# Kernel tuning notes

Hardware: AMD Instinct MI355X
Metric: run time of the kernel (lower is better)

The kernel has to match this reference:

```python
import jax, jax.numpy as jnp
import numpy as np

N_NODES = 50000
N_EDGES = 800000
D = 128
N_LAYERS = 3  # n_layers=2 -> 3 attention layers


def setup_inputs() -> dict:
    key = jax.random.key(0)
    ks = jax.random.split(key, 7)
    x = jax.random.normal(ks[0], (N_NODES, D), dtype=jnp.float32)
    edge_src = jax.random.randint(ks[1], (N_EDGES,), 0, N_NODES)
    edge_dst = jax.random.randint(ks[2], (N_EDGES,), 0, N_NODES)
    # Linear weights stored as [in, out] (equivalent to torch W.T)
    lin_w = jax.random.normal(ks[3], (N_LAYERS, D, D), dtype=jnp.float32) / np.sqrt(D)
    lin_b = jax.random.normal(ks[4], (N_LAYERS, D), dtype=jnp.float32) * 0.01
    attn_w = jax.random.normal(ks[5], (N_LAYERS, 2 * D), dtype=jnp.float32) / np.sqrt(2 * D)
    attn_b = jax.random.normal(ks[6], (N_LAYERS,), dtype=jnp.float32) * 0.01
    return {"x": x, "edge_src": edge_src, "edge_dst": edge_dst,
            "lin_w": lin_w, "lin_b": lin_b, "attn_w": attn_w, "attn_b": attn_b}


def reference(x, edge_src, edge_dst, lin_w, lin_b, attn_w, attn_b):
    n = x.shape[0]
    h = x
    for l in range(N_LAYERS):
        # h = leaky_relu(linear(x), 0.2)
        h = jax.nn.leaky_relu(h @ lin_w[l] + lin_b[l], negative_slope=0.2)
        f = h.shape[1]
        # e_ij = attn(cat(h_i, h_j)) -> split the attn weight into left/right halves
        s_left = h @ attn_w[l, :f]   # [N]
        s_right = h @ attn_w[l, f:]  # [N]
        e = s_left[edge_src] + s_right[edge_dst] + attn_b[l]  # [E]
        # sparse softmax over dim=1: normalize per source row i
        m = jax.ops.segment_max(e, edge_src, num_segments=n)
        ex = jnp.exp(e - m[edge_src])
        denom = jax.ops.segment_sum(ex, edge_src, num_segments=n)
        alpha = ex / denom[edge_src]  # [E]
        # h2[i] += h[j] * alpha_ij
        h2 = jax.ops.segment_sum(h[edge_dst] * alpha[:, None], edge_src, num_segments=n)
        h = jax.nn.relu(h2)  # self.activation
    return h
```

## Files before the change

### kernel.cpp

```cpp
#include <hip/hip_runtime.h>
#include <math.h>

#define N_NODES 50000
#define N_EDGES 800000
#define D 128
#define N_LAYERS 3

#define FCHUNK 2048
#define NCHUNK ((N_EDGES + FCHUNK - 1) / FCHUNK)
#define GDIV 6250
#define SLOT 96
#define PREPB ((N_LAYERS * D * D) / 256)
#define LINB ((N_NODES + 63) / 64)

typedef _Float16 half8 __attribute__((ext_vector_type(8)));
typedef _Float16 half4 __attribute__((ext_vector_type(4)));
typedef float f32x4 __attribute__((ext_vector_type(4)));

__global__ __launch_bounds__(256) void prep_w_kernel(
    const float* __restrict__ W, _Float16* __restrict__ Wt)
{
    int idx = blockIdx.x * 256 + threadIdx.x;
    int l = idx >> 14, rem = idx & (D * D - 1);
    int k = rem >> 7, n = rem & 127;
    Wt[l * D * D + n * D + k] = (_Float16)W[idx];
}

template <bool F32IN, bool FUSEFILL>
__global__ __launch_bounds__(256) void linear_mfma_kernel(
    const void* __restrict__ Ain, const _Float16* __restrict__ Wt,
    const float* __restrict__ b, const float* __restrict__ awr,
    _Float16* __restrict__ hout, float* __restrict__ sr,
    const int* __restrict__ esrc, const int* __restrict__ edst,
    int* __restrict__ cnt, unsigned short* __restrict__ csr16)
{
    __shared__ _Float16 Wl[D * 130];

    if (FUSEFILL && blockIdx.x >= LINB) {
        int fi = blockIdx.x - LINB;
        int g = blockIdx.x & 7;
        int base = (fi >> 3) * FCHUNK;
        int ecnt = N_EDGES - base;
        if (ecnt > FCHUNK) ecnt = FCHUNK;
        unsigned glo = (unsigned)(g * GDIV);
        for (int i = threadIdx.x * 4; i < ecnt; i += 1024) {
            int4 s4 = *(const int4*)(esrc + base + i);
            int4 d4 = *(const int4*)(edst + base + i);
            int ss[4] = {s4.x, s4.y, s4.z, s4.w};
            int dd[4] = {d4.x, d4.y, d4.z, d4.w};
#pragma unroll
            for (int j = 0; j < 4; ++j) {
                if ((unsigned)ss[j] - glo < (unsigned)GDIV) {
                    int pos = atomicAdd(cnt + ss[j], 1);
                    if (pos < SLOT)
                        csr16[(size_t)ss[j] * SLOT + pos] = (unsigned short)dd[j];
                }
            }
        }
        return;
    }

    int tid = threadIdx.x;
    for (int j = tid * 8; j < D * D; j += 2048) {
        int n = j >> 7, k = j & 127;
        *(half8*)(&Wl[n * 130 + k]) = *(const half8*)(Wt + j);
    }
    __syncthreads();

    int wid = tid >> 6, lane = tid & 63;
    int m = lane & 15, q = lane >> 4;
    int rowbase = blockIdx.x * 64 + wid * 16;
    int row = rowbase + m;

    half8 a[4];
    if (row < N_NODES) {
        if (F32IN) {
            const float* ar = (const float*)Ain + (size_t)row * D;
#pragma unroll
            for (int s = 0; s < 4; ++s) {
                float4 lo = *(const float4*)(ar + s * 32 + q * 8);
                float4 hi = *(const float4*)(ar + s * 32 + q * 8 + 4);
                a[s][0] = (_Float16)lo.x; a[s][1] = (_Float16)lo.y;
                a[s][2] = (_Float16)lo.z; a[s][3] = (_Float16)lo.w;
                a[s][4] = (_Float16)hi.x; a[s][5] = (_Float16)hi.y;
                a[s][6] = (_Float16)hi.z; a[s][7] = (_Float16)hi.w;
            }
        } else {
            const _Float16* ar = (const _Float16*)Ain + (size_t)row * D;
#pragma unroll
            for (int s = 0; s < 4; ++s)
                a[s] = *(const half8*)(ar + s * 32 + q * 8);
        }
    } else {
#pragma unroll
        for (int s = 0; s < 4; ++s)
#pragma unroll
            for (int j = 0; j < 8; ++j) a[s][j] = (_Float16)0.f;
    }

    f32x4 acc[8];
#pragma unroll
    for (int t = 0; t < 8; ++t) acc[t] = (f32x4)(0.f);

#pragma unroll
    for (int s = 0; s < 4; ++s) {
#pragma unroll
        for (int t = 0; t < 8; ++t) {
            half8 bf = *(const half8*)(&Wl[(t * 16 + m) * 130 + s * 32 + q * 8]);
            acc[t] = __builtin_amdgcn_mfma_f32_16x16x32_f16(a[s], bf, acc[t], 0, 0, 0);
        }
    }

    float sp[4] = {0.f, 0.f, 0.f, 0.f};
#pragma unroll
    for (int t = 0; t < 8; ++t) {
        int col = t * 16 + m;
        float bc = b[col];
        float ac = awr[col];
#pragma unroll
        for (int r = 0; r < 4; ++r) {
            int orow = rowbase + q * 4 + r;
            float v = acc[t][r] + bc;
            v = v > 0.f ? v : 0.2f * v;
            sp[r] = fmaf(v, ac, sp[r]);
            if (orow < N_NODES)
                hout[(size_t)orow * D + col] = (_Float16)v;
        }
    }
#pragma unroll
    for (int r = 0; r < 4; ++r) {
#pragma unroll
        for (int o = 1; o < 16; o <<= 1)
            sp[r] += __shfl_xor(sp[r], o, 64);
    }
    if (m == 0) {
#pragma unroll
        for (int r = 0; r < 4; ++r) {
            int orow = rowbase + q * 4 + r;
            if (orow < N_NODES) sr[orow] = sp[r];
        }
    }
}

__global__ __launch_bounds__(256, 8) void gather_kernel(
    const int* __restrict__ cnt, const unsigned short* __restrict__ csr16,
    const float* __restrict__ sr, const _Float16* __restrict__ h,
    _Float16* __restrict__ out16, float* __restrict__ out32)
{
    __shared__ int plds[4][2 * SLOT + 8];
    int wid = threadIdx.x >> 6, lane = threadIdx.x & 63;
    int half = lane >> 5, sl = lane & 31;
    int n = blockIdx.x * 4 + wid;
    int deg = cnt[n];
    if (deg > SLOT) deg = SLOT;
    const unsigned short* ce = csr16 + (size_t)n * SLOT;
    int* prow = plds[wid];

    float ev[2];
    float m = -INFINITY;
#pragma unroll
    for (int t = 0; t < 2; ++t) {
        int k = t * 64 + lane;
        if (k < deg) {
            int d = ce[k];
            prow[2 * k] = d << 8;
            float e = sr[d];
            ev[t] = e;
            m = fmaxf(m, e);
        }
    }
    for (int o = 32; o > 0; o >>= 1) m = fmaxf(m, __shfl_xor(m, o, 64));

    float s = 0.f;
#pragma unroll
    for (int t = 0; t < 2; ++t) {
        int k = t * 64 + lane;
        if (k < deg) {
            float a = __expf(ev[t] - m);
            prow[2 * k + 1] = __float_as_int(a);
            s += a;
        }
    }
    for (int o = 32; o > 0; o >>= 1) s += __shfl_xor(s, o, 64);
    float inv = (deg > 0) ? 1.f / s : 0.f;

    float acc0 = 0.f, acc1 = 0.f, acc2 = 0.f, acc3 = 0.f;
    const char* hb = (const char*)h + sl * 8;
    int k = 0;
    int deg8 = deg & ~7;
    for (; k < deg8; k += 8) {
        int2 p0 = *(const int2*)(prow + 2 * (k + half));
        int2 p1 = *(const int2*)(prow + 2 * (k + 2 + half));
        int2 p2 = *(const int2*)(prow + 2 * (k + 4 + half));
        int2 p3 = *(const int2*)(prow + 2 * (k + 6 + half));
        half4 h0 = *(const half4*)(hb + p0.x);
        half4 h1 = *(const half4*)(hb + p1.x);
        half4 h2 = *(const half4*)(hb + p2.x);
        half4 h3 = *(const half4*)(hb + p3.x);
        float a0 = __int_as_float(p0.y);
        float a1 = __int_as_float(p1.y);
        float a2 = __int_as_float(p2.y);
        float a3 = __int_as_float(p3.y);
        acc0 = fmaf((float)h0[0], a0, acc0);
        acc1 = fmaf((float)h0[1], a0, acc1);
        acc2 = fmaf((float)h0[2], a0, acc2);
        acc3 = fmaf((float)h0[3], a0, acc3);
        acc0 = fmaf((float)h1[0], a1, acc0);
        acc1 = fmaf((float)h1[1], a1, acc1);
        acc2 = fmaf((float)h1[2], a1, acc2);
        acc3 = fmaf((float)h1[3], a1, acc3);
        acc0 = fmaf((float)h2[0], a2, acc0);
        acc1 = fmaf((float)h2[1], a2, acc1);
        acc2 = fmaf((float)h2[2], a2, acc2);
        acc3 = fmaf((float)h2[3], a2, acc3);
        acc0 = fmaf((float)h3[0], a3, acc0);
        acc1 = fmaf((float)h3[1], a3, acc1);
        acc2 = fmaf((float)h3[2], a3, acc2);
        acc3 = fmaf((float)h3[3], a3, acc3);
    }
    for (; k < deg; k += 2) {
        int kk = k + half;
        int2 p = (kk < deg) ? *(const int2*)(prow + 2 * kk) : make_int2(0, 0);
        half4 hv = *(const half4*)(hb + p.x);
        float a = __int_as_float(p.y);
        acc0 = fmaf((float)hv[0], a, acc0);
        acc1 = fmaf((float)hv[1], a, acc1);
        acc2 = fmaf((float)hv[2], a, acc2);
        acc3 = fmaf((float)hv[3], a, acc3);
    }

    acc0 += __shfl_xor(acc0, 32, 64);
    acc1 += __shfl_xor(acc1, 32, 64);
    acc2 += __shfl_xor(acc2, 32, 64);
    acc3 += __shfl_xor(acc3, 32, 64);

    if (half == 0) {
        float r0 = fmaxf(acc0 * inv, 0.f);
        float r1 = fmaxf(acc1 * inv, 0.f);
        float r2 = fmaxf(acc2 * inv, 0.f);
        float r3 = fmaxf(acc3 * inv, 0.f);
        if (out16) {
            half4 o;
            o[0] = (_Float16)r0; o[1] = (_Float16)r1;
            o[2] = (_Float16)r2; o[3] = (_Float16)r3;
            *(half4*)(out16 + (size_t)n * D + sl * 4) = o;
        } else {
            float4 o = make_float4(r0, r1, r2, r3);
            *(float4*)(out32 + (size_t)n * D + sl * 4) = o;
        }
    }
}

extern "C" void kernel_launch(void* const* d_in, const int* in_sizes, int n_in,
                              void* d_out, int out_size, void* d_ws, size_t ws_size,
                              hipStream_t stream)
{
    const float* x      = (const float*)d_in[0];
    const int*   esrc   = (const int*)d_in[1];
    const int*   edst   = (const int*)d_in[2];
    const float* lin_w  = (const float*)d_in[3];
    const float* lin_b  = (const float*)d_in[4];
    const float* attn_w = (const float*)d_in[5];
    float* out = (float*)d_out;

    char* ws = (char*)d_ws;
    _Float16*       h16A  = (_Float16*)(ws);
    _Float16*       h16B  = (_Float16*)(ws + 12800000);
    float*          sr    = (float*)(ws + 25600000);
    int*            cnt   = (int*)(ws + 25800000);
    unsigned short* csr16 = (unsigned short*)(ws + 26000000);
    _Float16*       Wt16  = (_Float16*)(ws + 35600000);

    hipMemsetAsync(cnt, 0, N_NODES * sizeof(int), stream);
    prep_w_kernel<<<PREPB, 256, 0, stream>>>(lin_w, Wt16);

    for (int l = 0; l < N_LAYERS; ++l) {
        bool last = (l == N_LAYERS - 1);
        if (l == 0)
            linear_mfma_kernel<true, true><<<LINB + NCHUNK * 8, 256, 0, stream>>>(
                x, Wt16, lin_b, attn_w + D, h16A, sr,
                esrc, edst, cnt, csr16);
        else
            linear_mfma_kernel<false, false><<<LINB, 256, 0, stream>>>(
                h16B, Wt16 + (size_t)l * D * D, lin_b + (size_t)l * D,
                attn_w + (size_t)l * 2 * D + D, h16A, sr,
                nullptr, nullptr, nullptr, nullptr);
        gather_kernel<<<N_NODES / 4, 256, 0, stream>>>(
            cnt, csr16, sr, h16A,
            last ? (_Float16*)nullptr : h16B, last ? out : nullptr);
    }
}
```

Measured before the change: 261.2 us.

## Slice node features into 16-column planes and gather per slice

Stores the fp16 hidden features as eight column slices of 16 halves per node, so each slice array is smaller and more likely to stay resident in cache. The gather kernel now processes one slice per block, with each wave covering five nodes and 16 edges in parallel via shuffles instead of LDS. The softmax over edges is recomputed once for every slice, so that work is done eight times. The degree cap drops from 96 to 64, which truncates neighbors for high-degree nodes and may change results.

```diff
diff --git a/kernel.cpp b/kernel.cpp
--- a/kernel.cpp
+++ b/kernel.cpp
@@ -12,6 +12,11 @@
 #define SLOT 96
 #define PREPB ((N_LAYERS * D * D) / 256)
 #define LINB ((N_NODES + 63) / 64)
+
+#define SLICE_ELEMS (N_NODES * 16)
+#define NPW 5
+#define NGRP (N_NODES / (4 * NPW))
+#define GBLK (NGRP * 8)
 
 typedef _Float16 half8 __attribute__((ext_vector_type(8)));
 typedef _Float16 half4 __attribute__((ext_vector_type(4)));
@@ -86,10 +91,12 @@
                 a[s][6] = (_Float16)hi.z; a[s][7] = (_Float16)hi.w;
             }
         } else {
-            const _Float16* ar = (const _Float16*)Ain + (size_t)row * D;
-#pragma unroll
-            for (int s = 0; s < 4; ++s)
-                a[s] = *(const half8*)(ar + s * 32 + q * 8);
+            const _Float16* ar = (const _Float16*)Ain;
+#pragma unroll
+            for (int s = 0; s < 4; ++s) {
+                int sl = 2 * s + (q >> 1);
+                a[s] = *(const half8*)(ar + (size_t)sl * SLICE_ELEMS + row * 16 + (q & 1) * 8);
+            }
         }
     } else {
 #pragma unroll
@@ -124,7 +131,7 @@
             v = v > 0.f ? v : 0.2f * v;
             sp[r] = fmaf(v, ac, sp[r]);
             if (orow < N_NODES)
-                hout[(size_t)orow * D + col] = (_Float16)v;
+                hout[(size_t)t * SLICE_ELEMS + orow * 16 + m] = (_Float16)v;
         }
     }
 #pragma unroll
@@ -142,111 +149,67 @@
     }
 }
 
-__global__ __launch_bounds__(256, 8) void gather_kernel(
+__global__ __launch_bounds__(256) void gather_sliced_kernel(
     const int* __restrict__ cnt, const unsigned short* __restrict__ csr16,
     const float* __restrict__ sr, const _Float16* __restrict__ h,
     _Float16* __restrict__ out16, float* __restrict__ out32)
 {
-    __shared__ int plds[4][2 * SLOT + 8];
+    int s = blockIdx.x & 7;
+    int grp = blockIdx.x >> 3;
     int wid = threadIdx.x >> 6, lane = threadIdx.x & 63;
-    int half = lane >> 5, sl = lane & 31;
-    int n = blockIdx.x * 4 + wid;
-    int deg = cnt[n];
-    if (deg > SLOT) deg = SLOT;
-    const unsigned short* ce = csr16 + (size_t)n * SLOT;
-    int* prow = plds[wid];
-
-    float ev[2];
-    float m = -INFINITY;
-#pragma unroll
-    for (int t = 0; t < 2; ++t) {
-        int k = t * 64 + lane;
-        if (k < deg) {
-            int d = ce[k];
-            prow[2 * k] = d << 8;
-            float e = sr[d];
-            ev[t] = e;
-            m = fmaxf(m, e);
-        }
-    }
-    for (int o = 32; o > 0; o >>= 1) m = fmaxf(m, __shfl_xor(m, o, 64));
-
-    float s = 0.f;
-#pragma unroll
-    for (int t = 0; t < 2; ++t) {
-        int k = t * 64 + lane;
-        if (k < deg) {
-            float a = __expf(ev[t] - m);
-            prow[2 * k + 1] = __float_as_int(a);
-            s += a;
-        }
-    }
-    for (int o = 32; o > 0; o >>= 1) s += __shfl_xor(s, o, 64);
-    float inv = (deg > 0) ? 1.f / s : 0.f;
-
-    float acc0 = 0.f, acc1 = 0.f, acc2 = 0.f, acc3 = 0.f;
-    const char* hb = (const char*)h + sl * 8;
-    int k = 0;
-    int deg8 = deg & ~7;
-    for (; k < deg8; k += 8) {
-        int2 p0 = *(const int2*)(prow + 2 * (k + half));
-        int2 p1 = *(const int2*)(prow + 2 * (k + 2 + half));
-        int2 p2 = *(const int2*)(prow + 2 * (k + 4 + half));
-        int2 p3 = *(const int2*)(prow + 2 * (k + 6 + half));
-        half4 h0 = *(const half4*)(hb + p0.x);
-        half4 h1 = *(const half4*)(hb + p1.x);
-        half4 h2 = *(const half4*)(hb + p2.x);
-        half4 h3 = *(const half4*)(hb + p3.x);
-        float a0 = __int_as_float(p0.y);
-        float a1 = __int_as_float(p1.y);
-        float a2 = __int_as_float(p2.y);
-        float a3 = __int_as_float(p3.y);
-        acc0 = fmaf((float)h0[0], a0, acc0);
-        acc1 = fmaf((float)h0[1], a0, acc1);
-        acc2 = fmaf((float)h0[2], a0, acc2);
-        acc3 = fmaf((float)h0[3], a0, acc3);
-        acc0 = fmaf((float)h1[0], a1, acc0);
-        acc1 = fmaf((float)h1[1], a1, acc1);
-        acc2 = fmaf((float)h1[2], a1, acc2);
-        acc3 = fmaf((float)h1[3], a1, acc3);
-        acc0 = fmaf((float)h2[0], a2, acc0);
-        acc1 = fmaf((float)h2[1], a2, acc1);
-        acc2 = fmaf((float)h2[2], a2, acc2);
-        acc3 = fmaf((float)h2[3], a2, acc3);
-        acc0 = fmaf((float)h3[0], a3, acc0);
-        acc1 = fmaf((float)h3[1], a3, acc1);
-        acc2 = fmaf((float)h3[2], a3, acc2);
-        acc3 = fmaf((float)h3[3], a3, acc3);
-    }
-    for (; k < deg; k += 2) {
-        int kk = k + half;
-        int2 p = (kk < deg) ? *(const int2*)(prow + 2 * kk) : make_int2(0, 0);
-        half4 hv = *(const half4*)(hb + p.x);
-        float a = __int_as_float(p.y);
-        acc0 = fmaf((float)hv[0], a, acc0);
-        acc1 = fmaf((float)hv[1], a, acc1);
-        acc2 = fmaf((float)hv[2], a, acc2);
-        acc3 = fmaf((float)hv[3], a, acc3);
-    }
-
-    acc0 += __shfl_xor(acc0, 32, 64);
-    acc1 += __shfl_xor(acc1, 32, 64);
-    acc2 += __shfl_xor(acc2, 32, 64);
-    acc3 += __shfl_xor(acc3, 32, 64);
-
-    if (half == 0) {
-        float r0 = fmaxf(acc0 * inv, 0.f);
-        float r1 = fmaxf(acc1 * inv, 0.f);
-        float r2 = fmaxf(acc2 * inv, 0.f);
-        float r3 = fmaxf(acc3 * inv, 0.f);
-        if (out16) {
-            half4 o;
-            o[0] = (_Float16)r0; o[1] = (_Float16)r1;
-            o[2] = (_Float16)r2; o[3] = (_Float16)r3;
-            *(half4*)(out16 + (size_t)n * D + sl * 4) = o;
-        } else {
-            float4 o = make_float4(r0, r1, r2, r3);
-            *(float4*)(out32 + (size_t)n * D + sl * 4) = o;
+    int e = lane >> 2, c = lane & 3;
+    const _Float16* hs = h + (size_t)s * SLICE_ELEMS;
+    int nbase = grp * (4 * NPW) + wid * NPW;
+
+    for (int nn = 0; nn < NPW; ++nn) {
+        int n = nbase + nn;
+        if (n >= N_NODES) break;
+        int deg = cnt[n];
+        if (deg > 64) deg = 64;
+        const unsigned short* ce = csr16 + (size_t)n * SLOT;
+
+        int dl = 0;
+        float ev = -INFINITY;
+        if (lane < deg) { dl = ce[lane]; ev = sr[dl]; }
+        float m = ev;
+        for (int o = 32; o > 0; o >>= 1) m = fmaxf(m, __shfl_xor(m, o, 64));
+        float a = (lane < deg) ? __expf(ev - m) : 0.f;
+        float ssum = a;
+        for (int o = 32; o > 0; o >>= 1) ssum += __shfl_xor(ssum, o, 64);
+        float al = (deg > 0) ? a / ssum : 0.f;
+
+        float acc0 = 0.f, acc1 = 0.f, acc2 = 0.f, acc3 = 0.f;
+        for (int k = 0; k < deg; k += 16) {
+            int es = k + e;
+            int d = __shfl(dl, es, 64);
+            float av = __shfl(al, es, 64);
+            half4 hv = *(const half4*)(hs + (size_t)d * 16 + c * 4);
+            acc0 = fmaf((float)hv[0], av, acc0);
+            acc1 = fmaf((float)hv[1], av, acc1);
+            acc2 = fmaf((float)hv[2], av, acc2);
+            acc3 = fmaf((float)hv[3], av, acc3);
+        }
+#pragma unroll
+        for (int o = 4; o < 64; o <<= 1) {
+            acc0 += __shfl_xor(acc0, o, 64);
+            acc1 += __shfl_xor(acc1, o, 64);
+            acc2 += __shfl_xor(acc2, o, 64);
+            acc3 += __shfl_xor(acc3, o, 64);
+        }
+        if (e == 0) {
+            float r0 = fmaxf(acc0, 0.f);
+            float r1 = fmaxf(acc1, 0.f);
+            float r2 = fmaxf(acc2, 0.f);
+            float r3 = fmaxf(acc3, 0.f);
+            if (out16) {
+                half4 o4;
+                o4[0] = (_Float16)r0; o4[1] = (_Float16)r1;
+                o4[2] = (_Float16)r2; o4[3] = (_Float16)r3;
+                *(half4*)(out16 + (size_t)s * SLICE_ELEMS + n * 16 + c * 4) = o4;
+            } else {
+                float4 o4 = make_float4(r0, r1, r2, r3);
+                *(float4*)(out32 + (size_t)n * D + s * 16 + c * 4) = o4;
+            }
         }
     }
 }
@@ -285,7 +248,7 @@
                 h16B, Wt16 + (size_t)l * D * D, lin_b + (size_t)l * D,
                 attn_w + (size_t)l * 2 * D + D, h16A, sr,
                 nullptr, nullptr, nullptr, nullptr);
-        gather_kernel<<<N_NODES / 4, 256, 0, stream>>>(
+        gather_sliced_kernel<<<GBLK, 256, 0, stream>>>(
             cnt, csr16, sr, h16A,
             last ? (_Float16*)nullptr : h16B, last ? out : nullptr);
     }
```

After: 554.7 us. 112% more time.

## Move CSR fill out of first linear kernel into fused weight-prep kernel

Applied to the files above, without the earlier changes.

The edge-bucketing CSR fill moves out of the layer-0 linear kernel and into the weight-conversion kernel, which now runs as one combined launch before the layers. The fill chunk size doubles, so each fill block covers twice as many edges and fewer blocks are launched. The linear kernel loses its template branch and extra arguments, which may lower register pressure. The cost is that the fill no longer overlaps the first matmul; it now runs alongside the much smaller weight-prep work.

```diff
diff --git a/kernel.cpp b/kernel.cpp
--- a/kernel.cpp
+++ b/kernel.cpp
@@ -6,7 +6,7 @@
 #define D 128
 #define N_LAYERS 3
 
-#define FCHUNK 2048
+#define FCHUNK 4096
 #define NCHUNK ((N_EDGES + FCHUNK - 1) / FCHUNK)
 #define GDIV 6250
 #define SLOT 96
@@ -17,49 +17,45 @@
 typedef _Float16 half4 __attribute__((ext_vector_type(4)));
 typedef float f32x4 __attribute__((ext_vector_type(4)));
 
-__global__ __launch_bounds__(256) void prep_w_kernel(
+__global__ __launch_bounds__(256, 8) void fill_prep_kernel(
+    const int* __restrict__ src, const int* __restrict__ dst,
+    int* __restrict__ cnt, unsigned short* __restrict__ csr16,
     const float* __restrict__ W, _Float16* __restrict__ Wt)
 {
-    int idx = blockIdx.x * 256 + threadIdx.x;
-    int l = idx >> 14, rem = idx & (D * D - 1);
-    int k = rem >> 7, n = rem & 127;
-    Wt[l * D * D + n * D + k] = (_Float16)W[idx];
-}
-
-template <bool F32IN, bool FUSEFILL>
+    if (blockIdx.x >= NCHUNK * 8) {
+        int idx = (blockIdx.x - NCHUNK * 8) * 256 + threadIdx.x;
+        int l = idx >> 14, rem = idx & (D * D - 1);
+        int k = rem >> 7, n = rem & 127;
+        Wt[l * D * D + n * D + k] = (_Float16)W[idx];
+        return;
+    }
+    int g = blockIdx.x & 7;
+    int base = (blockIdx.x >> 3) * FCHUNK;
+    int ecnt = N_EDGES - base;
+    if (ecnt > FCHUNK) ecnt = FCHUNK;
+    unsigned glo = (unsigned)(g * GDIV);
+    for (int i = threadIdx.x * 4; i < ecnt; i += 1024) {
+        int4 s4 = *(const int4*)(src + base + i);
+        int4 d4 = *(const int4*)(dst + base + i);
+        int ss[4] = {s4.x, s4.y, s4.z, s4.w};
+        int dd[4] = {d4.x, d4.y, d4.z, d4.w};
+#pragma unroll
+        for (int j = 0; j < 4; ++j) {
+            if ((unsigned)ss[j] - glo < (unsigned)GDIV) {
+                int pos = atomicAdd(cnt + ss[j], 1);
+                if (pos < SLOT) csr16[(size_t)ss[j] * SLOT + pos] = (unsigned short)dd[j];
+            }
+        }
+    }
+}
+
+template <bool F32IN>
 __global__ __launch_bounds__(256) void linear_mfma_kernel(
     const void* __restrict__ Ain, const _Float16* __restrict__ Wt,
     const float* __restrict__ b, const float* __restrict__ awr,
-    _Float16* __restrict__ hout, float* __restrict__ sr,
-    const int* __restrict__ esrc, const int* __restrict__ edst,
-    int* __restrict__ cnt, unsigned short* __restrict__ csr16)
+    _Float16* __restrict__ hout, float* __restrict__ sr)
 {
     __shared__ _Float16 Wl[D * 130];
-
-    if (FUSEFILL && blockIdx.x >= LINB) {
-        int fi = blockIdx.x - LINB;
-        int g = blockIdx.x & 7;
-        int base = (fi >> 3) * FCHUNK;
-        int ecnt = N_EDGES - base;
-        if (ecnt > FCHUNK) ecnt = FCHUNK;
-        unsigned glo = (unsigned)(g * GDIV);
-        for (int i = threadIdx.x * 4; i < ecnt; i += 1024) {
-            int4 s4 = *(const int4*)(esrc + base + i);
-            int4 d4 = *(const int4*)(edst + base + i);
-            int ss[4] = {s4.x, s4.y, s4.z, s4.w};
-            int dd[4] = {d4.x, d4.y, d4.z, d4.w};
-#pragma unroll
-            for (int j = 0; j < 4; ++j) {
-                if ((unsigned)ss[j] - glo < (unsigned)GDIV) {
-                    int pos = atomicAdd(cnt + ss[j], 1);
-                    if (pos < SLOT)
-                        csr16[(size_t)ss[j] * SLOT + pos] = (unsigned short)dd[j];
-                }
-            }
-        }
-        return;
-    }
-
     int tid = threadIdx.x;
     for (int j = tid * 8; j < D * D; j += 2048) {
         int n = j >> 7, k = j & 127;
@@ -272,19 +268,19 @@
     _Float16*       Wt16  = (_Float16*)(ws + 35600000);
 
     hipMemsetAsync(cnt, 0, N_NODES * sizeof(int), stream);
-    prep_w_kernel<<<PREPB, 256, 0, stream>>>(lin_w, Wt16);
+    fill_prep_kernel<<<NCHUNK * 8 + PREPB, 256, 0, stream>>>(
+        esrc, edst, cnt, csr16, lin_w, Wt16);
 
     for (int l = 0; l < N_LAYERS; ++l) {
+        const void* A = (l == 0) ? (const void*)x : (const void*)h16B;
+        if (l == 0)
+            linear_mfma_kernel<true><<<LINB, 256, 0, stream>>>(
+                A, Wt16, lin_b, attn_w + D, h16A, sr);
+        else
+            linear_mfma_kernel<false><<<LINB, 256, 0, stream>>>(
+                A, Wt16 + (size_t)l * D * D, lin_b + (size_t)l * D,
+                attn_w + (size_t)l * 2 * D + D, h16A, sr);
         bool last = (l == N_LAYERS - 1);
-        if (l == 0)
-            linear_mfma_kernel<true, true><<<LINB + NCHUNK * 8, 256, 0, stream>>>(
-                x, Wt16, lin_b, attn_w + D, h16A, sr,
-                esrc, edst, cnt, csr16);
-        else
-            linear_mfma_kernel<false, false><<<LINB, 256, 0, stream>>>(
-                h16B, Wt16 + (size_t)l * D * D, lin_b + (size_t)l * D,
-                attn_w + (size_t)l * 2 * D + D, h16A, sr,
-                nullptr, nullptr, nullptr, nullptr);
         gather_kernel<<<N_NODES / 4, 256, 0, stream>>>(
             cnt, csr16, sr, h16A,
             last ? (_Float16*)nullptr : h16B, last ? out : nullptr);
```

New measurement: 268.3 us. +2.7%, slower.

## Halve linear-kernel weight LDS tile, fold memset into prep, enlarge fill chunks

Applied to the files above, without the earlier changes.

The linear MFMA kernel now stages weights in two 64-column halves, which halves shared memory per block, and adds a launch-bounds occupancy hint to fit more blocks per CU. The cnt memset is folded into the weight-prep kernel, removing one launch. The CSR fill chunk size is doubled, so fewer fill blocks each do more work. The cost is an extra LDS reload and two more barriers per block, with some risk of register pressure from the occupancy hint.

```diff
diff --git a/kernel.cpp b/kernel.cpp
--- a/kernel.cpp
+++ b/kernel.cpp
@@ -6,40 +6,45 @@
 #define D 128
 #define N_LAYERS 3
 
-#define FCHUNK 2048
+#define FCHUNK 4096
 #define NCHUNK ((N_EDGES + FCHUNK - 1) / FCHUNK)
 #define GDIV 6250
 #define SLOT 96
 #define PREPB ((N_LAYERS * D * D) / 256)
+#define CNTB ((N_NODES + 255) / 256)
 #define LINB ((N_NODES + 63) / 64)
 
 typedef _Float16 half8 __attribute__((ext_vector_type(8)));
 typedef _Float16 half4 __attribute__((ext_vector_type(4)));
 typedef float f32x4 __attribute__((ext_vector_type(4)));
 
-__global__ __launch_bounds__(256) void prep_w_kernel(
-    const float* __restrict__ W, _Float16* __restrict__ Wt)
-{
-    int idx = blockIdx.x * 256 + threadIdx.x;
-    int l = idx >> 14, rem = idx & (D * D - 1);
-    int k = rem >> 7, n = rem & 127;
-    Wt[l * D * D + n * D + k] = (_Float16)W[idx];
+__global__ __launch_bounds__(256) void prep_kernel(
+    const float* __restrict__ W, _Float16* __restrict__ Wt, int* __restrict__ cnt)
+{
+    if (blockIdx.x < PREPB) {
+        int idx = blockIdx.x * 256 + threadIdx.x;
+        int l = idx >> 14, rem = idx & (D * D - 1);
+        int k = rem >> 7, n = rem & 127;
+        Wt[l * D * D + n * D + k] = (_Float16)W[idx];
+    } else {
+        int i = (blockIdx.x - PREPB) * 256 + threadIdx.x;
+        if (i < N_NODES) cnt[i] = 0;
+    }
 }
 
 template <bool F32IN, bool FUSEFILL>
-__global__ __launch_bounds__(256) void linear_mfma_kernel(
+__global__ __launch_bounds__(256, 6) void linear_mfma_kernel(
     const void* __restrict__ Ain, const _Float16* __restrict__ Wt,
     const float* __restrict__ b, const float* __restrict__ awr,
     _Float16* __restrict__ hout, float* __restrict__ sr,
     const int* __restrict__ esrc, const int* __restrict__ edst,
     int* __restrict__ cnt, unsigned short* __restrict__ csr16)
 {
-    __shared__ _Float16 Wl[D * 130];
+    __shared__ _Float16 Wl[64 * 130];
 
     if (FUSEFILL && blockIdx.x >= LINB) {
-        int fi = blockIdx.x - LINB;
         int g = blockIdx.x & 7;
-        int base = (fi >> 3) * FCHUNK;
+        int base = ((blockIdx.x - LINB) >> 3) * FCHUNK;
         int ecnt = N_EDGES - base;
         if (ecnt > FCHUNK) ecnt = FCHUNK;
         unsigned glo = (unsigned)(g * GDIV);
@@ -61,12 +66,6 @@
     }
 
     int tid = threadIdx.x;
-    for (int j = tid * 8; j < D * D; j += 2048) {
-        int n = j >> 7, k = j & 127;
-        *(half8*)(&Wl[n * 130 + k]) = *(const half8*)(Wt + j);
-    }
-    __syncthreads();
-
     int wid = tid >> 6, lane = tid & 63;
     int m = lane & 15, q = lane >> 4;
     int rowbase = blockIdx.x * 64 + wid * 16;
@@ -103,12 +102,21 @@
     for (int t = 0; t < 8; ++t) acc[t] = (f32x4)(0.f);
 
 #pragma unroll
-    for (int s = 0; s < 4; ++s) {
-#pragma unroll
-        for (int t = 0; t < 8; ++t) {
-            half8 bf = *(const half8*)(&Wl[(t * 16 + m) * 130 + s * 32 + q * 8]);
-            acc[t] = __builtin_amdgcn_mfma_f32_16x16x32_f16(a[s], bf, acc[t], 0, 0, 0);
-        }
+    for (int hh = 0; hh < 2; ++hh) {
+        for (int j = tid * 8; j < 64 * D; j += 2048) {
+            int n = j >> 7, k = j & 127;
+            *(half8*)(&Wl[n * 130 + k]) = *(const half8*)(Wt + (hh * 64 + n) * D + k);
+        }
+        __syncthreads();
+#pragma unroll
+        for (int s = 0; s < 4; ++s) {
+#pragma unroll
+            for (int t = 0; t < 4; ++t) {
+                half8 bf = *(const half8*)(&Wl[(t * 16 + m) * 130 + s * 32 + q * 8]);
+                acc[hh * 4 + t] = __builtin_amdgcn_mfma_f32_16x16x32_f16(a[s], bf, acc[hh * 4 + t], 0, 0, 0);
+            }
+        }
+        __syncthreads();
     }
 
     float sp[4] = {0.f, 0.f, 0.f, 0.f};
@@ -271,8 +279,7 @@
     unsigned short* csr16 = (unsigned short*)(ws + 26000000);
     _Float16*       Wt16  = (_Float16*)(ws + 35600000);
 
-    hipMemsetAsync(cnt, 0, N_NODES * sizeof(int), stream);
-    prep_w_kernel<<<PREPB, 256, 0, stream>>>(lin_w, Wt16);
+    prep_kernel<<<PREPB + CNTB, 256, 0, stream>>>(lin_w, Wt16, cnt);
 
     for (int l = 0; l < N_LAYERS; ++l) {
         bool last = (l == N_LAYERS - 1);
```

Result: no change. 262.4 us (+0.5%).
